# Kernel tuning notes

Measured on AMD Instinct MI355X. Metric: run time of the kernel, lower is better.

Reference implementation:

```python
import jax, jax.numpy as jnp
import numpy as np

NC = 80          # classes
REG_MAX = 16     # DFL bins
NK = 51          # 17*3 keypoint channels
KPT_SHAPE = (17, 3)
MAX_DET = 100
CONF_THRES = 0.25
STRIDES = (8, 16, 32)


def _conv1x1(f, w, b):
    # f: (B,C,H,W), w: (O,C), b: (O,) -> (B,O,H,W)
    return jnp.einsum('bchw,oc->bohw', f, w) + b[None, :, None, None]


def _make_anchors(shapes, strides, offset=0.5):
    pts, sts = [], []
    for (h, w), s in zip(shapes, strides):
        sx = jnp.arange(w, dtype=jnp.float32) + offset
        sy = jnp.arange(h, dtype=jnp.float32) + offset
        gy, gx = jnp.meshgrid(sy, sx, indexing='ij')
        pts.append(jnp.stack([gx, gy], -1).reshape(-1, 2))
        sts.append(jnp.full((h * w, 1), float(s), jnp.float32))
    # transposed as in _new_inference: anchors (2,A), strides (1,A)
    return jnp.concatenate(pts, 0).T, jnp.concatenate(sts, 0).T


def setup_inputs() -> dict:
    key = jax.random.key(0)
    ks = jax.random.split(key, 16)
    ch = (128, 256, 512)
    hw = ((80, 80), (40, 40), (20, 20))
    d = {}
    for i, (c, (h, w)) in enumerate(zip(ch, hw)):
        d[f'x{i}'] = jax.random.normal(ks[i], (16, c, h, w), jnp.float32)
    k = 3
    for name, oc in (('cv2', 4 * REG_MAX), ('cv3', NC), ('cv4', NK)):
        for i, c in enumerate(ch):
            d[f'{name}_w{i}'] = jax.random.normal(ks[k], (oc, c), jnp.float32) * 0.02
            d[f'{name}_b{i}'] = jnp.zeros((oc,), jnp.float32)
            k += 1
    return d


def reference(x0, x1, x2,
              cv2_w0, cv2_b0, cv2_w1, cv2_b1, cv2_w2, cv2_b2,
              cv3_w0, cv3_b0, cv3_w1, cv3_b1, cv3_w2, cv3_b2,
              cv4_w0, cv4_b0, cv4_w1, cv4_b1, cv4_w2, cv4_b2):
    feats = [x0, x1, x2]
    cv2 = [(cv2_w0, cv2_b0), (cv2_w1, cv2_b1), (cv2_w2, cv2_b2)]
    cv3 = [(cv3_w0, cv3_b0), (cv3_w1, cv3_b1), (cv3_w2, cv3_b2)]
    cv4 = [(cv4_w0, cv4_b0), (cv4_w1, cv4_b1), (cv4_w2, cv4_b2)]
    bs = x0.shape[0]

    # keypoint branch: cat over levels -> (bs, nk, A)
    kpt = jnp.concatenate(
        [_conv1x1(f, w, b).reshape(bs, NK, -1) for f, (w, b) in zip(feats, cv4)], -1)
    # box+cls branch -> (bs, 4*reg_max+nc, A)
    xcat = jnp.concatenate(
        [jnp.concatenate([_conv1x1(f, *cv2[i]), _conv1x1(f, *cv3[i])], 1).reshape(bs, 4 * REG_MAX + NC, -1)
         for i, f in enumerate(feats)], -1)
    box, cls = xcat[:, :4 * REG_MAX], xcat[:, 4 * REG_MAX:]

    shapes = [(f.shape[2], f.shape[3]) for f in feats]
    anchors, strides = _make_anchors(shapes, STRIDES)  # (2,A), (1,A)
    A = anchors.shape[1]

    # DFL decode: softmax over reg_max bins, expectation w/ arange weights
    p = jax.nn.softmax(box.reshape(bs, 4, REG_MAX, A), axis=2)
    dist = jnp.einsum('bfra,r->bfa', p, jnp.arange(REG_MAX, dtype=jnp.float32))
    lt, rb = dist[:, :2], dist[:, 2:]
    x1y1 = anchors[None] - lt
    x2y2 = anchors[None] + rb
    # xywh box coding, scaled by strides
    dbox = jnp.concatenate([(x1y1 + x2y2) * 0.5, x2y2 - x1y1], 1) * strides[None]  # (bs,4,A)

    # keypoint decode (Pose.kpts_decode, ndim==3)
    y = kpt.reshape(bs, KPT_SHAPE[0], KPT_SHAPE[1], A)
    kxy = (y[:, :, :2] * 2.0 + (anchors[None, None] - 0.5)) * strides[None, None]
    kv = jax.nn.sigmoid(y[:, :, 2:3])
    pred_kpts = jnp.concatenate([kxy, kv], 2).reshape(bs, NK, A).transpose(0, 2, 1)  # (bs,A,nk)

    # EfficientIdxNMS_TRT stand-in: sigmoid scores (score_activation=1),
    # class-agnostic deterministic top-k selection by best class score.
    scores = jax.nn.sigmoid(cls.transpose(0, 2, 1))  # (bs,A,nc)
    max_s = scores.max(-1)
    cls_id = jnp.argmax(scores, -1)
    top_s, top_i = jax.lax.top_k(max_s, MAX_DET)     # (bs,MAX_DET)
    num_dets = (top_s > CONF_THRES).sum(-1).astype(jnp.int32)[:, None]
    det_boxes = jnp.take_along_axis(dbox.transpose(0, 2, 1), top_i[..., None], 1)  # (bs,MAX_DET,4)
    det_classes = jnp.take_along_axis(cls_id, top_i, 1).astype(jnp.int32)
    # irregular keypoint gather via det indices (the pred_kpts[bs_indices, det_indices] step)
    det_kpts = jnp.take_along_axis(pred_kpts, top_i[..., None], 1).reshape(bs, MAX_DET, *KPT_SHAPE)
    return num_dets, det_boxes, top_s, det_classes, det_kpts
```

## Files before the change

kernel.cpp:

```cpp
#include <hip/hip_runtime.h>
#include <hip/hip_bf16.h>

#define NC 80
#define NK 51
#define REG_MAX 16
#define MAX_DET 100
#define A_TOT 8400
#define BS 16

#define OUT_NUM 0
#define OUT_BOX 16
#define OUT_SCORE (16 + 16*MAX_DET*4)
#define OUT_CLASS (OUT_SCORE + 16*MAX_DET)
#define OUT_KPT (OUT_CLASS + 16*MAX_DET)

static __device__ __forceinline__ unsigned long long mk_key(unsigned u, int a) {
    return ((unsigned long long)u << 32) | (unsigned)(0x7FFFFFFF - a);
}

__global__ __launch_bounds__(512, 4) void scores_fused(
    const float* __restrict__ x0, const float* __restrict__ x1, const float* __restrict__ x2,
    const float* __restrict__ w0, const float* __restrict__ w1, const float* __restrict__ w2,
    const float* __restrict__ bias0, const float* __restrict__ bias1, const float* __restrict__ bias2,
    float* __restrict__ max_s,
    int* __restrict__ cls_id)
{
    __shared__ float fs[32 * 256];

    int bid = blockIdx.x;
    const float *x, *w, *bias; int C, A, a_off, b, tile;
    if (bid < 32) {
        x = x2; w = w2; bias = bias2; C = 512; A = 400; a_off = 8000;
        b = bid >> 1; tile = bid & 1;
    } else if (bid < 144) {
        int r = bid - 32;
        x = x1; w = w1; bias = bias1; C = 256; A = 1600; a_off = 6400;
        b = r / 7; tile = r - b * 7;
    } else {
        int r = bid - 144;
        x = x0; w = w0; bias = bias0; C = 128; A = 6400; a_off = 0;
        b = r / 25; tile = r - b * 25;
    }
    int a0 = tile * 256;

    int t = threadIdx.x;
    int lane = t & 63;
    int lane4 = lane * 4;
    int wv = __builtin_amdgcn_readfirstlane(t >> 6);
    int oc0 = wv * 10;

    float acc[10][4];
#pragma unroll
    for (int j = 0; j < 10; ++j) {
        float bv = bias[oc0 + j];
#pragma unroll
        for (int an = 0; an < 4; ++an) acc[j][an] = bv;
    }

    const float* xb = x + (long)b * C * A;
    int nchunk = C >> 5;

    float4 r[4];
#pragma unroll
    for (int i = 0; i < 4; ++i) {
        int idx = t + i * 512;
        int c = idx >> 6;
        int aa = a0 + ((idx & 63) << 2);
        if (aa > A - 4) aa = A - 4;
        r[i] = *(const float4*)(xb + (long)c * A + aa);
    }

    for (int kc = 0; kc < nchunk; ++kc) {
#pragma unroll
        for (int i = 0; i < 4; ++i)
            *(float4*)&fs[(t + i * 512) * 4] = r[i];
        if (kc + 1 < nchunk) {
#pragma unroll
            for (int i = 0; i < 4; ++i) {
                int idx = t + i * 512;
                int c = (kc + 1) * 32 + (idx >> 6);
                int aa = a0 + ((idx & 63) << 2);
                if (aa > A - 4) aa = A - 4;
                r[i] = *(const float4*)(xb + (long)c * A + aa);
            }
        }
        __syncthreads();

        const float* wbase = w + oc0 * C + kc * 32;
#pragma unroll 1
        for (int c4 = 0; c4 < 32; c4 += 4) {
            float4 f0 = *(const float4*)&fs[(c4 + 0) * 256 + lane4];
            float4 f1 = *(const float4*)&fs[(c4 + 1) * 256 + lane4];
            float4 f2 = *(const float4*)&fs[(c4 + 2) * 256 + lane4];
            float4 f3 = *(const float4*)&fs[(c4 + 3) * 256 + lane4];
#pragma unroll
            for (int j = 0; j < 10; ++j) {
                float4 wj = *(const float4*)(wbase + j * C + c4);
                acc[j][0] = fmaf(wj.x, f0.x, acc[j][0]);
                acc[j][0] = fmaf(wj.y, f1.x, acc[j][0]);
                acc[j][0] = fmaf(wj.z, f2.x, acc[j][0]);
                acc[j][0] = fmaf(wj.w, f3.x, acc[j][0]);
                acc[j][1] = fmaf(wj.x, f0.y, acc[j][1]);
                acc[j][1] = fmaf(wj.y, f1.y, acc[j][1]);
                acc[j][1] = fmaf(wj.z, f2.y, acc[j][1]);
                acc[j][1] = fmaf(wj.w, f3.y, acc[j][1]);
                acc[j][2] = fmaf(wj.x, f0.z, acc[j][2]);
                acc[j][2] = fmaf(wj.y, f1.z, acc[j][2]);
                acc[j][2] = fmaf(wj.z, f2.z, acc[j][2]);
                acc[j][2] = fmaf(wj.w, f3.z, acc[j][2]);
                acc[j][3] = fmaf(wj.x, f0.w, acc[j][3]);
                acc[j][3] = fmaf(wj.y, f1.w, acc[j][3]);
                acc[j][3] = fmaf(wj.z, f2.w, acc[j][3]);
                acc[j][3] = fmaf(wj.w, f3.w, acc[j][3]);
            }
        }
        __syncthreads();
    }

    float* rm = fs;
    int*   ri = (int*)(fs + 2048);
#pragma unroll
    for (int an = 0; an < 4; ++an) {
        float m = acc[0][an]; int mi = 0;
#pragma unroll
        for (int j = 1; j < 10; ++j)
            if (acc[j][an] > m) { m = acc[j][an]; mi = j; }
        rm[wv * 256 + lane4 + an] = m;
        ri[wv * 256 + lane4 + an] = mi + oc0;
    }
    __syncthreads();

    if (t < 256) {
        float bm = rm[t]; int bi = ri[t];
#pragma unroll
        for (int v = 1; v < 8; ++v) {
            float om = rm[v * 256 + t];
            if (om > bm) { bm = om; bi = ri[v * 256 + t]; }
        }
        int ga = a0 + t;
        if (ga < A) {
            max_s[b * A_TOT + a_off + ga] = 1.0f / (1.0f + expf(-bm));
            cls_id[b * A_TOT + a_off + ga] = bi;
        }
    }
}

__global__ __launch_bounds__(1024) void topk_kernel(
    const float* __restrict__ max_s,
    const int* __restrict__ cls_id,
    float* __restrict__ out,
    int* __restrict__ top_idx)
{
    int b = blockIdx.x;
    int t = threadIdx.x;
    int wv = t >> 6;

    __shared__ unsigned hist[16 * 256];
    __shared__ unsigned suffix[256];
    __shared__ int tieIdx[A_TOT];
    __shared__ unsigned long long highKeys[128];
    __shared__ unsigned long long finalKeys[128];
    __shared__ int wmin[16];
    __shared__ unsigned s_prefix;
    __shared__ int s_k, s_selD, s_nHigh, s_nTie, s_cnt, s_bcast;

    unsigned u[9];
    bool val[9];
#pragma unroll
    for (int i = 0; i < 9; ++i) {
        int a = t + i * 1024;
        val[i] = (a < A_TOT);
        u[i] = val[i] ? __float_as_uint(max_s[b * A_TOT + a]) : 0u;
    }

    if (t == 0) { s_prefix = 0; s_k = MAX_DET; s_nHigh = 0; s_nTie = 0; s_cnt = 0; }

    for (int pass = 0; pass < 4; ++pass) {
#pragma unroll
        for (int j = 0; j < 4; ++j) hist[t + j * 1024] = 0;
        if (t == 0) s_selD = 0;
        __syncthreads();

        unsigned pre = s_prefix;
        int k = s_k;
        int shHi = 32 - 8 * pass;
        int shD = 24 - 8 * pass;
#pragma unroll
        for (int i = 0; i < 9; ++i) {
            if (val[i]) {
                bool cand = (pass == 0) ? true : ((u[i] >> shHi) == pre);
                if (cand)
                    atomicAdd(&hist[(wv << 8) + ((u[i] >> shD) & 0xFF)], 1u);
            }
        }
        __syncthreads();

        if (t < 256) {
            unsigned s = 0;
#pragma unroll
            for (int w = 0; w < 16; ++w) s += hist[(w << 8) + t];
            suffix[t] = s;
        }
        __syncthreads();
        for (int off = 1; off < 256; off <<= 1) {
            unsigned v = 0;
            if (t < 256) v = suffix[t] + ((t + off < 256) ? suffix[t + off] : 0u);
            __syncthreads();
            if (t < 256) suffix[t] = v;
            __syncthreads();
        }
        if (t < 256 && suffix[t] >= (unsigned)k) atomicMax(&s_selD, t);
        __syncthreads();
        if (t == 0) {
            int d = s_selD;
            s_k = k - ((d < 255) ? (int)suffix[d + 1] : 0);
            s_prefix = (pre << 8) | (unsigned)d;
        }
        __syncthreads();
    }

    unsigned cut = s_prefix;
    int r = s_k;

#pragma unroll
    for (int i = 0; i < 9; ++i) {
        if (val[i]) {
            int a = t + i * 1024;
            if (u[i] > cut) {
                int p = atomicAdd(&s_nHigh, 1);
                highKeys[p] = mk_key(u[i], a);
            } else if (u[i] == cut) {
                int p = atomicAdd(&s_nTie, 1);
                tieIdx[p] = a;
            }
        }
    }
    __syncthreads();
    int m = s_nHigh;
    int nt = s_nTie;

    if (t < 128) finalKeys[t] = 0ull;
    __syncthreads();
    if (t < m) finalKeys[t] = highKeys[t];

    if (nt == r) {
        if (t < nt) finalKeys[m + t] = mk_key(cut, tieIdx[t]);
        __syncthreads();
    } else {
        __syncthreads();
        for (int j = 0; j < r; ++j) {
            int mn = 0x7FFFFFFF;
            for (int p = t; p < nt; p += 1024) mn = min(mn, tieIdx[p]);
            for (int off = 32; off > 0; off >>= 1) mn = min(mn, __shfl_down(mn, off, 64));
            if ((t & 63) == 0) wmin[wv] = mn;
            __syncthreads();
            if (t == 0) {
                int v = wmin[0];
#pragma unroll
                for (int w = 1; w < 16; ++w) v = min(v, wmin[w]);
                s_bcast = v;
                finalKeys[m + j] = mk_key(cut, v);
            }
            __syncthreads();
            int v = s_bcast;
            for (int p = t; p < nt; p += 1024)
                if (tieIdx[p] == v) tieIdx[p] = 0x7FFFFFFF;
            __syncthreads();
        }
    }

    for (int ksz = 2; ksz <= 128; ksz <<= 1) {
        for (int j = ksz >> 1; j > 0; j >>= 1) {
            if (t < 128) {
                int ixj = t ^ j;
                if (ixj > t) {
                    bool desc = ((t & ksz) == 0);
                    unsigned long long x = finalKeys[t], y = finalKeys[ixj];
                    bool sw = desc ? (x < y) : (x > y);
                    if (sw) { finalKeys[t] = y; finalKeys[ixj] = x; }
                }
            }
            __syncthreads();
        }
    }

    if (t < MAX_DET) {
        unsigned long long kk = finalKeys[t];
        float sc = __uint_as_float((unsigned)(kk >> 32));
        int a = 0x7FFFFFFF - (int)(kk & 0xFFFFFFFFull);
        out[OUT_SCORE + b * MAX_DET + t] = sc;
        out[OUT_CLASS + b * MAX_DET + t] = (float)cls_id[b * A_TOT + a];
        top_idx[b * MAX_DET + t] = a;
        if (sc > 0.25f) atomicAdd(&s_cnt, 1);
    }
    __syncthreads();
    if (t == 0) out[OUT_NUM + b] = (float)s_cnt;
}

__global__ __launch_bounds__(128) void decode_kernel(
    const float* __restrict__ x0, const float* __restrict__ x1, const float* __restrict__ x2,
    const float* __restrict__ w2_0, const float* __restrict__ b2_0,
    const float* __restrict__ w2_1, const float* __restrict__ b2_1,
    const float* __restrict__ w2_2, const float* __restrict__ b2_2,
    const float* __restrict__ w4_0, const float* __restrict__ b4_0,
    const float* __restrict__ w4_1, const float* __restrict__ b4_1,
    const float* __restrict__ w4_2, const float* __restrict__ b4_2,
    const int* __restrict__ top_idx,
    float* __restrict__ out)
{
    int b = blockIdx.y;
    int k = blockIdx.x;
    int a = top_idx[b * MAX_DET + k];

    const float* x; const float* w2; const float* bb2; const float* w4; const float* bb4;
    int C, A, W, a_local; float stride;
    if (a < 6400)      { x = x0; C = 128; A = 6400; W = 80; stride = 8.0f;  a_local = a;        w2 = w2_0; bb2 = b2_0; w4 = w4_0; bb4 = b4_0; }
    else if (a < 8000) { x = x1; C = 256; A = 1600; W = 40; stride = 16.0f; a_local = a - 6400; w2 = w2_1; bb2 = b2_1; w4 = w4_1; bb4 = b4_1; }
    else               { x = x2; C = 512; A = 400;  W = 20; stride = 32.0f; a_local = a - 8000; w2 = w2_2; bb2 = b2_2; w4 = w4_2; bb4 = b4_2; }

    __shared__ float fs[512];
    __shared__ float logits[64];
    __shared__ float kraw[NK];
    __shared__ float dist[4];

    int t = threadIdx.x;
    for (int c = t; c < C; c += 128)
        fs[c] = x[((long)b * C + c) * A + a_local];
    __syncthreads();

    if (t < 64 + NK) {
        const float* wrow; float acc;
        if (t < 64) { wrow = w2 + t * C; acc = bb2[t]; }
        else        { wrow = w4 + (t - 64) * C; acc = bb4[t - 64]; }
        for (int c = 0; c < C; ++c) acc = fmaf(wrow[c], fs[c], acc);
        if (t < 64) logits[t] = acc;
        else        kraw[t - 64] = acc;
    }
    __syncthreads();

    if (t < 4) {
        float mx = logits[t * 16];
#pragma unroll
        for (int r = 1; r < 16; ++r) mx = fmaxf(mx, logits[t * 16 + r]);
        float se = 0.0f, sw = 0.0f;
#pragma unroll
        for (int r = 0; r < 16; ++r) {
            float e = expf(logits[t * 16 + r] - mx);
            se += e; sw += e * (float)r;
        }
        dist[t] = sw / se;
    }
    __syncthreads();

    float ax = (float)(a_local % W) + 0.5f;
    float ay = (float)(a_local / W) + 0.5f;

    if (t == 0) {
        float x1c = ax - dist[0], y1c = ay - dist[1];
        float x2c = ax + dist[2], y2c = ay + dist[3];
        float* ob = out + OUT_BOX + ((long)b * MAX_DET + k) * 4;
        ob[0] = (x1c + x2c) * 0.5f * stride;
        ob[1] = (y1c + y2c) * 0.5f * stride;
        ob[2] = (x2c - x1c) * stride;
        ob[3] = (y2c - y1c) * stride;
    }
    if (t < 17) {
        float vx = kraw[t * 3], vy = kraw[t * 3 + 1], vv = kraw[t * 3 + 2];
        float gx = ax - 0.5f, gy = ay - 0.5f;
        float* ok = out + OUT_KPT + (((long)b * MAX_DET + k) * 17 + t) * 3;
        ok[0] = (vx * 2.0f + gx) * stride;
        ok[1] = (vy * 2.0f + gy) * stride;
        ok[2] = 1.0f / (1.0f + expf(-vv));
    }
}

extern "C" void kernel_launch(void* const* d_in, const int* in_sizes, int n_in,
                              void* d_out, int out_size, void* d_ws, size_t ws_size,
                              hipStream_t stream) {
    const float* x0 = (const float*)d_in[0];
    const float* x1 = (const float*)d_in[1];
    const float* x2 = (const float*)d_in[2];
    const float* w2[3] = {(const float*)d_in[3], (const float*)d_in[5], (const float*)d_in[7]};
    const float* b2[3] = {(const float*)d_in[4], (const float*)d_in[6], (const float*)d_in[8]};
    const float* w3[3] = {(const float*)d_in[9], (const float*)d_in[11], (const float*)d_in[13]};
    const float* b3[3] = {(const float*)d_in[10], (const float*)d_in[12], (const float*)d_in[14]};
    const float* w4[3] = {(const float*)d_in[15], (const float*)d_in[17], (const float*)d_in[19]};
    const float* b4[3] = {(const float*)d_in[16], (const float*)d_in[18], (const float*)d_in[20]};

    float* out = (float*)d_out;

    float* ws_maxs = (float*)d_ws;
    int* ws_cls = (int*)(ws_maxs + BS * A_TOT);
    int* ws_top = (int*)(ws_cls + BS * A_TOT);

    scores_fused<<<dim3(544), 512, 0, stream>>>(
        x0, x1, x2, w3[0], w3[1], w3[2], b3[0], b3[1], b3[2], ws_maxs, ws_cls);
    topk_kernel<<<dim3(BS), 1024, 0, stream>>>(ws_maxs, ws_cls, out, ws_top);
    decode_kernel<<<dim3(MAX_DET, BS), 128, 0, stream>>>(
        x0, x1, x2,
        w2[0], b2[0], w2[1], b2[1], w2[2], b2[2],
        w4[0], b4[0], w4[1], b4[1], w4[2], b4[2],
        ws_top, out);
}
```

Before: 374.3 us.

## Restructure class-score GEMM to 256 threads with shared-memory weights and vectorize decode dot

The class-score kernel drops from 512 to 256 threads per block. Each wave now computes 20 output channels instead of 10, and the weight slice for each 32-channel chunk is staged in shared memory rather than read from global memory per thread. The register prefetch double-buffering of the feature tile is removed in favour of a direct load-then-sync per chunk. The decode kernel's per-thread dot product is vectorized with float4 loads and unrolled. Doubling the accumulators raises register pressure and lowers occupancy, and losing the prefetch exposes global load latency.

```diff
diff --git a/kernel.cpp b/kernel.cpp
--- a/kernel.cpp
+++ b/kernel.cpp
@@ -18,7 +18,7 @@
     return ((unsigned long long)u << 32) | (unsigned)(0x7FFFFFFF - a);
 }
 
-__global__ __launch_bounds__(512, 4) void scores_fused(
+__global__ __launch_bounds__(256) void scores_fused(
     const float* __restrict__ x0, const float* __restrict__ x1, const float* __restrict__ x2,
     const float* __restrict__ w0, const float* __restrict__ w1, const float* __restrict__ w2,
     const float* __restrict__ bias0, const float* __restrict__ bias1, const float* __restrict__ bias2,
@@ -26,6 +26,7 @@
     int* __restrict__ cls_id)
 {
     __shared__ float fs[32 * 256];
+    __shared__ float wsh[80 * 32];
 
     int bid = blockIdx.x;
     const float *x, *w, *bias; int C, A, a_off, b, tile;
@@ -47,11 +48,11 @@
     int lane = t & 63;
     int lane4 = lane * 4;
     int wv = __builtin_amdgcn_readfirstlane(t >> 6);
-    int oc0 = wv * 10;
-
-    float acc[10][4];
-#pragma unroll
-    for (int j = 0; j < 10; ++j) {
+    int oc0 = wv * 20;
+
+    float acc[20][4];
+#pragma unroll
+    for (int j = 0; j < 20; ++j) {
         float bv = bias[oc0 + j];
 #pragma unroll
         for (int an = 0; an < 4; ++an) acc[j][an] = bv;
@@ -60,33 +61,29 @@
     const float* xb = x + (long)b * C * A;
     int nchunk = C >> 5;
 
-    float4 r[4];
-#pragma unroll
-    for (int i = 0; i < 4; ++i) {
-        int idx = t + i * 512;
-        int c = idx >> 6;
-        int aa = a0 + ((idx & 63) << 2);
-        if (aa > A - 4) aa = A - 4;
-        r[i] = *(const float4*)(xb + (long)c * A + aa);
-    }
-
     for (int kc = 0; kc < nchunk; ++kc) {
-#pragma unroll
-        for (int i = 0; i < 4; ++i)
-            *(float4*)&fs[(t + i * 512) * 4] = r[i];
-        if (kc + 1 < nchunk) {
-#pragma unroll
-            for (int i = 0; i < 4; ++i) {
-                int idx = t + i * 512;
-                int c = (kc + 1) * 32 + (idx >> 6);
-                int aa = a0 + ((idx & 63) << 2);
-                if (aa > A - 4) aa = A - 4;
-                r[i] = *(const float4*)(xb + (long)c * A + aa);
-            }
-        }
-        __syncthreads();
-
-        const float* wbase = w + oc0 * C + kc * 32;
+        __syncthreads();
+#pragma unroll
+        for (int i = 0; i < 8; ++i) {
+            int idx = t + i * 256;
+            int c = idx >> 6;
+            int q = (idx & 63) * 4;
+            int aa = a0 + q; if (aa > A - 4) aa = A - 4;
+            float4 v = *(const float4*)(xb + (long)(kc * 32 + c) * A + aa);
+            *(float4*)(&fs[c * 256 + q]) = v;
+        }
+#pragma unroll
+        for (int i = 0; i < 3; ++i) {
+            int idx = t + i * 256;
+            if (idx < 640) {
+                int oc = idx >> 3;
+                int q = (idx & 7) * 4;
+                float4 v = *(const float4*)(w + oc * C + kc * 32 + q);
+                *(float4*)(&wsh[oc * 32 + q]) = v;
+            }
+        }
+        __syncthreads();
+
 #pragma unroll 1
         for (int c4 = 0; c4 < 32; c4 += 4) {
             float4 f0 = *(const float4*)&fs[(c4 + 0) * 256 + lane4];
@@ -94,8 +91,8 @@
             float4 f2 = *(const float4*)&fs[(c4 + 2) * 256 + lane4];
             float4 f3 = *(const float4*)&fs[(c4 + 3) * 256 + lane4];
 #pragma unroll
-            for (int j = 0; j < 10; ++j) {
-                float4 wj = *(const float4*)(wbase + j * C + c4);
+            for (int j = 0; j < 20; ++j) {
+                float4 wj = *(const float4*)(&wsh[(oc0 + j) * 32 + c4]);
                 acc[j][0] = fmaf(wj.x, f0.x, acc[j][0]);
                 acc[j][0] = fmaf(wj.y, f1.x, acc[j][0]);
                 acc[j][0] = fmaf(wj.z, f2.x, acc[j][0]);
@@ -114,26 +111,32 @@
                 acc[j][3] = fmaf(wj.w, f3.w, acc[j][3]);
             }
         }
-        __syncthreads();
-    }
-
+    }
+
+    float m[4]; int mi[4];
+#pragma unroll
+    for (int an = 0; an < 4; ++an) { m[an] = acc[0][an]; mi[an] = 0; }
+#pragma unroll
+    for (int j = 1; j < 20; ++j) {
+#pragma unroll
+        for (int an = 0; an < 4; ++an)
+            if (acc[j][an] > m[an]) { m[an] = acc[j][an]; mi[an] = j; }
+    }
+
+    __syncthreads();
     float* rm = fs;
-    int*   ri = (int*)(fs + 2048);
+    int*   ri = (int*)(fs + 1024);
 #pragma unroll
     for (int an = 0; an < 4; ++an) {
-        float m = acc[0][an]; int mi = 0;
-#pragma unroll
-        for (int j = 1; j < 10; ++j)
-            if (acc[j][an] > m) { m = acc[j][an]; mi = j; }
-        rm[wv * 256 + lane4 + an] = m;
-        ri[wv * 256 + lane4 + an] = mi + oc0;
+        rm[wv * 256 + lane4 + an] = m[an];
+        ri[wv * 256 + lane4 + an] = mi[an] + oc0;
     }
     __syncthreads();
 
     if (t < 256) {
         float bm = rm[t]; int bi = ri[t];
 #pragma unroll
-        for (int v = 1; v < 8; ++v) {
+        for (int v = 1; v < 4; ++v) {
             float om = rm[v * 256 + t];
             if (om > bm) { bm = om; bi = ri[v * 256 + t]; }
         }
@@ -332,7 +335,21 @@
         const float* wrow; float acc;
         if (t < 64) { wrow = w2 + t * C; acc = bb2[t]; }
         else        { wrow = w4 + (t - 64) * C; acc = bb4[t - 64]; }
-        for (int c = 0; c < C; ++c) acc = fmaf(wrow[c], fs[c], acc);
+#pragma unroll 4
+        for (int c = 0; c < C; c += 8) {
+            float4 wa = *(const float4*)(wrow + c);
+            float4 wb = *(const float4*)(wrow + c + 4);
+            float4 fa = *(const float4*)&fs[c];
+            float4 fb = *(const float4*)&fs[c + 4];
+            acc = fmaf(wa.x, fa.x, acc);
+            acc = fmaf(wa.y, fa.y, acc);
+            acc = fmaf(wa.z, fa.z, acc);
+            acc = fmaf(wa.w, fa.w, acc);
+            acc = fmaf(wb.x, fb.x, acc);
+            acc = fmaf(wb.y, fb.y, acc);
+            acc = fmaf(wb.z, fb.z, acc);
+            acc = fmaf(wb.w, fb.w, acc);
+        }
         if (t < 64) logits[t] = acc;
         else        kraw[t - 64] = acc;
     }
@@ -393,7 +410,7 @@
     int* ws_cls = (int*)(ws_maxs + BS * A_TOT);
     int* ws_top = (int*)(ws_cls + BS * A_TOT);
 
-    scores_fused<<<dim3(544), 512, 0, stream>>>(
+    scores_fused<<<dim3(544), 256, 0, stream>>>(
         x0, x1, x2, w3[0], w3[1], w3[2], b3[0], b3[1], b3[2], ws_maxs, ws_cls);
     topk_kernel<<<dim3(BS), 1024, 0, stream>>>(ws_maxs, ws_cls, out, ws_top);
     decode_kernel<<<dim3(MAX_DET, BS), 128, 0, stream>>>(
```

New measurement: 355.4 us. 1.05x faster.
